# Kernel tuning notes

Hardware: AMD Instinct MI355X
Metric: run time of the kernel (lower is better)

## Reference

```python
import jax, jax.numpy as jnp
import numpy as np

WINDOW = (-100000, 100000)
BINWIDTHS = np.array([100, 200, 500, 1000, 2000, 5000], dtype=np.int64)  # S=6 scales
NBINS = (WINDOW[1] - WINDOW[0]) // BINWIDTHS + 1                        # bins per scale
BINSHIFTS = WINDOW[0] // BINWIDTHS                                       # floor div (exact here)
BINCUMSTARTS = np.concatenate([np.zeros(1, dtype=np.int64), np.cumsum(NBINS)[:-1]])
N_WEIGHTS = int(NBINS.sum())  # 3746

F, C, R, D = 100000, 2, 500, 100


def setup_inputs() -> dict:
    key = jax.random.key(0)
    k1, k2, k3, k4 = jax.random.split(key, 4)
    # coordinates span the full window, including negatives
    coordinates = jax.random.randint(k1, (F, C), 0, WINDOW[1] - WINDOW[0]) + WINDOW[0]
    region_ids = jax.random.randint(k2, (F,), 0, R)
    W = jax.random.normal(k3, (R, N_WEIGHTS, D), dtype=jnp.float32) * 0.02
    bias = jax.random.normal(k4, (R, D), dtype=jnp.float32) * 0.02
    return {"coordinates": coordinates, "region_ids": region_ids, "W": W, "bias": bias}


def reference(coordinates, region_ids, W, bias):
    bw = jnp.asarray(BINWIDTHS)          # [S]
    shifts = jnp.asarray(BINSHIFTS)      # [S]
    starts = jnp.asarray(BINCUMSTARTS)   # [S]
    coords = jnp.clip(coordinates, WINDOW[0], WINDOW[1] - 1)  # [F,C]
    c = coords[None]  # [1,F,C], broadcast vs [S,1,1]
    bin_ix = c // bw[:, None, None] - shifts[:, None, None] + starts[:, None, None]  # [S,F,C]
    alpha = (c % bw[:, None, None]).astype(jnp.float32) / bw[:, None, None].astype(jnp.float32)  # [S,F,C]
    r = region_ids[None, :, None]  # [1,F,1] broadcasts with bin_ix
    w0 = W[r, bin_ix]              # [S,F,C,D] gather
    w1 = W[r, bin_ix + 1]          # [S,F,C,D] gather
    out = (jnp.einsum('sfcd,sfc->fd', w0, 1.0 - alpha)
           + jnp.einsum('sfcd,sfc->fd', w1, alpha)
           + bias[region_ids])     # [F,D]
    return out
```

## Files before the change

kernel.cpp:

```cpp
#include <hip/hip_runtime.h>

#define F_N 100000
#define C_N 2
#define R_N 500
#define D_N 100
#define NW  3746
#define D4  25


__global__ __launch_bounds__(256) void spline_enc_kernel(
    const int*   __restrict__ coords,
    const int*   __restrict__ region_ids,
    const float* __restrict__ W,
    const float* __restrict__ bias,
    float*       __restrict__ out)
{
    const int gid = blockIdx.x * blockDim.x + threadIdx.x;
    const int f = gid / D4;
    const int j = gid % D4;
    if (f >= F_N) return;

    const int r = region_ids[f];

    int c0 = coords[2 * f];
    int c1 = coords[2 * f + 1];
    c0 = min(max(c0, -100000), 99999);
    c1 = min(max(c1, -100000), 99999);
    const unsigned u0 = (unsigned)(c0 + 100000);
    const unsigned u1 = (unsigned)(c1 + 100000);

    const float4* __restrict__ Wr =
        (const float4*)(W + (size_t)r * ((size_t)NW * D_N));
    const float4* __restrict__ br =
        (const float4*)(bias + (size_t)r * D_N);

    float4 acc = br[j];

    const unsigned bws[6]   = {100u, 200u, 500u, 1000u, 2000u, 5000u};
    const int      starts[6] = {0, 2001, 3002, 3403, 3604, 3705};

#pragma unroll
    for (int s = 0; s < 6; ++s) {
        const unsigned bw = bws[s];
        const float inv_bw = 1.0f / (float)bw;
        const int st = starts[s];
#pragma unroll
        for (int c = 0; c < 2; ++c) {
            const unsigned u = (c == 0) ? u0 : u1;
            const unsigned q = u / bw;
            const unsigned rem = u - q * bw;
            const float alpha = (float)rem * inv_bw;
            const float oma = 1.0f - alpha;
            const size_t row = (size_t)(q + (unsigned)st) * D4 + j;
            const float4 w0 = Wr[row];
            const float4 w1 = Wr[row + D4];
            acc.x = fmaf(w0.x, oma, acc.x);
            acc.y = fmaf(w0.y, oma, acc.y);
            acc.z = fmaf(w0.z, oma, acc.z);
            acc.w = fmaf(w0.w, oma, acc.w);
            acc.x = fmaf(w1.x, alpha, acc.x);
            acc.y = fmaf(w1.y, alpha, acc.y);
            acc.z = fmaf(w1.z, alpha, acc.z);
            acc.w = fmaf(w1.w, alpha, acc.w);
        }
    }

    ((float4*)out)[(size_t)f * D4 + j] = acc;
}

extern "C" void kernel_launch(void* const* d_in, const int* in_sizes, int n_in,
                              void* d_out, int out_size, void* d_ws, size_t ws_size,
                              hipStream_t stream) {
    const int*   coords     = (const int*)d_in[0];
    const int*   region_ids = (const int*)d_in[1];
    const float* W          = (const float*)d_in[2];
    const float* bias       = (const float*)d_in[3];
    float*       out        = (float*)d_out;

    const int total = F_N * D4;
    const int block = 256;
    const int grid  = (total + block - 1) / block;
    spline_enc_kernel<<<grid, block, 0, stream>>>(coords, region_ids, W, bias, out);
}
```

Measured before the change: 944.2 us.

## Sort features by region before gather to improve weight cache locality

```diff
diff --git a/kernel.cpp b/kernel.cpp
--- a/kernel.cpp
+++ b/kernel.cpp
@@ -6,20 +6,53 @@
 #define D_N 100
 #define NW  3746
 #define D4  25
+#define RPAD 512
 
+
+
+__global__ void zero_kernel(int* __restrict__ counts, int* __restrict__ cursor) {
+    int t = threadIdx.x;
+    if (t < RPAD) { counts[t] = 0; cursor[t] = 0; }
+}
+
+__global__ void count_kernel(const int* __restrict__ region_ids, int* __restrict__ counts) {
+    int f = blockIdx.x * blockDim.x + threadIdx.x;
+    if (f < F_N) atomicAdd(&counts[region_ids[f]], 1);
+}
+
+__global__ void scan_kernel(const int* __restrict__ counts, int* __restrict__ starts) {
+    if (threadIdx.x == 0 && blockIdx.x == 0) {
+        int acc = 0;
+        for (int r = 0; r < R_N; ++r) { starts[r] = acc; acc += counts[r]; }
+    }
+}
+
+__global__ void scatter_kernel(const int* __restrict__ region_ids,
+                               const int* __restrict__ starts,
+                               int* __restrict__ cursor,
+                               int* __restrict__ sorted_idx) {
+    int f = blockIdx.x * blockDim.x + threadIdx.x;
+    if (f < F_N) {
+        int r = region_ids[f];
+        int pos = starts[r] + atomicAdd(&cursor[r], 1);
+        sorted_idx[pos] = f;
+    }
+}
 
 __global__ __launch_bounds__(256) void spline_enc_kernel(
     const int*   __restrict__ coords,
     const int*   __restrict__ region_ids,
     const float* __restrict__ W,
     const float* __restrict__ bias,
+    const int*   __restrict__ sorted_idx,
     float*       __restrict__ out)
 {
     const int gid = blockIdx.x * blockDim.x + threadIdx.x;
-    const int f = gid / D4;
-    const int j = gid % D4;
-    if (f >= F_N) return;
+    const int sp = gid / D4;
+    const int j  = gid % D4;
+    if (sp >= F_N) return;
 
+    const int f = sorted_idx[sp];
     const int r = region_ids[f];
 
     int c0 = coords[2 * f];
@@ -36,7 +69,7 @@
 
     float4 acc = br[j];
 
-    const unsigned bws[6]   = {100u, 200u, 500u, 1000u, 2000u, 5000u};
+    const unsigned bws[6]    = {100u, 200u, 500u, 1000u, 2000u, 5000u};
     const int      starts[6] = {0, 2001, 3002, 3403, 3604, 3705};
 
 #pragma unroll
@@ -77,8 +110,22 @@
     const float* bias       = (const float*)d_in[3];
     float*       out        = (float*)d_out;
 
+    char* ws = (char*)d_ws;
+    int* counts     = (int*)(ws + 0);
+    int* starts     = (int*)(ws + 2048);
+    int* cursor     = (int*)(ws + 4096);
+    int* sorted_idx = (int*)(ws + 8192);
+
+    const int blk = 256;
+    const int gF  = (F_N + blk - 1) / blk;
+
+    zero_kernel<<<1, RPAD, 0, stream>>>(counts, cursor);
+    count_kernel<<<gF, blk, 0, stream>>>(region_ids, counts);
+    scan_kernel<<<1, 64, 0, stream>>>(counts, starts);
+    scatter_kernel<<<gF, blk, 0, stream>>>(region_ids, starts, cursor, sorted_idx);
+
     const int total = F_N * D4;
-    const int block = 256;
-    const int grid  = (total + block - 1) / block;
-    spline_enc_kernel<<<grid, block, 0, stream>>>(coords, region_ids, W, bias, out);
+    const int grid  = (total + blk - 1) / blk;
+    spline_enc_kernel<<<grid, blk, 0, stream>>>(coords, region_ids, W, bias,
+                                                sorted_idx, out);
 }
```

After: 982.2 us. 1.04x slower.
